# Optimization experiments

Measured on AMD Instinct MI355X. Metric: run time of the kernel, lower is better.

## Reference

```python
import jax, jax.numpy as jnp
import numpy as np

D = 128      # d_single
DP = 64      # d_pair
H = 8        # nhead
DH = D // H  # head dim = 16
DO = 32      # outer proj dim


def layernorm(x, g, b, eps=1e-5):
    mu = jnp.mean(x, axis=-1, keepdims=True)
    var = jnp.var(x, axis=-1, keepdims=True)
    return (x - mu) * jax.lax.rsqrt(var + eps) * g + b


def setup_inputs() -> dict:
    key = jax.random.key(0)
    ks = jax.random.split(key, 16)
    B, L = 2, 320
    s = 0.02
    return {
        "x": jax.random.normal(ks[0], (B, L, D), jnp.float32),
        "z": jax.random.normal(ks[1], (B, L, L, DP), jnp.float32),
        "Wq": jax.random.normal(ks[2], (D, D), jnp.float32) * s,
        "Wk": jax.random.normal(ks[3], (D, D), jnp.float32) * s,
        "Wv": jax.random.normal(ks[4], (D, D), jnp.float32) * s,
        "Wb": jax.random.normal(ks[5], (DP, H), jnp.float32) * s,
        "Wo": jax.random.normal(ks[6], (D, D), jnp.float32) * s,
        "bo": jnp.zeros((D,), jnp.float32),
        "ln1_g": jnp.ones((D,), jnp.float32),
        "ln1_b": jnp.zeros((D,), jnp.float32),
        "W_ffn1": jax.random.normal(ks[7], (D, 4 * D), jnp.float32) * s,
        "b_ffn1": jnp.zeros((4 * D,), jnp.float32),
        "W_ffn2": jax.random.normal(ks[8], (4 * D, D), jnp.float32) * s,
        "b_ffn2": jnp.zeros((D,), jnp.float32),
        "ln2_g": jnp.ones((D,), jnp.float32),
        "ln2_b": jnp.zeros((D,), jnp.float32),
        "Wp1": jax.random.normal(ks[9], (D, DO), jnp.float32) * s,
        "bp1": jnp.zeros((DO,), jnp.float32),
        "Wp2": jax.random.normal(ks[10], (D, DO), jnp.float32) * s,
        "bp2": jnp.zeros((DO,), jnp.float32),
        "Wz": jax.random.normal(ks[11], (DO * DO, DP), jnp.float32) * s,
        "bz": jnp.zeros((DP,), jnp.float32),
        "lnp_g": jnp.ones((DP,), jnp.float32),
        "lnp_b": jnp.zeros((DP,), jnp.float32),
    }


def reference(x, z, Wq, Wk, Wv, Wb, Wo, bo, ln1_g, ln1_b,
              W_ffn1, b_ffn1, W_ffn2, b_ffn2, ln2_g, ln2_b,
              Wp1, bp1, Wp2, bp2, Wz, bz, lnp_g, lnp_b):
    B, L, _ = x.shape
    # --- pair-biased self-attention (dropout = identity in eval) ---
    xn = layernorm(x, ln1_g, ln1_b)
    q = (xn @ Wq).reshape(B, L, H, DH)
    k = (xn @ Wk).reshape(B, L, H, DH)
    v = (xn @ Wv).reshape(B, L, H, DH)
    bias = jnp.einsum('bijp,ph->bhij', z, Wb)                 # [B,H,L,L]
    scores = jnp.einsum('bihd,bjhd->bhij', q, k) / jnp.sqrt(jnp.float32(DH))
    probs = jax.nn.softmax(scores + bias, axis=-1)
    out = jnp.einsum('bhij,bjhd->bihd', probs, v).reshape(B, L, D)
    x = x + out @ Wo + bo
    # --- FFN ---
    xn2 = layernorm(x, ln2_g, ln2_b)
    h = jax.nn.gelu(xn2 @ W_ffn1 + b_ffn1, approximate=False)
    x = x + h @ W_ffn2 + b_ffn2
    # --- outer-product pair update ---
    p1 = x @ Wp1 + bp1                                        # [B,L,32]
    p2 = x @ Wp2 + bp2                                        # [B,L,32]
    # einsum('bic,bjd->bijcd') then flatten(-2) then GEMM with Wz
    Wz4 = Wz.reshape(DO, DO, DP)
    upd = jnp.einsum('bic,bjd,cdp->bijp', p1, p2, Wz4) + bz   # [B,L,L,DP]
    z = layernorm(z + upd, lnp_g, lnp_b)
    return (x, z)
```

## Files before the change

### kernel.cpp

```cpp
#include <hip/hip_runtime.h>
#include <math.h>

#define D   128
#define DP  64
#define H   8
#define DH  16
#define DO  32
#define NB  2
#define L   320
#define NR  (NB * L)

__global__ __launch_bounds__(256) void k1_ln_qkv(
    const float* __restrict__ x, const float* __restrict__ Wq,
    const float* __restrict__ Wk, const float* __restrict__ Wv,
    const float* __restrict__ g, const float* __restrict__ bb,
    float* __restrict__ qkv) {
  __shared__ float xs[2][D];
  __shared__ float stat[2][2];
  const int t = threadIdx.x;
  const int r0 = blockIdx.x * 2;
  const int row = t >> 7, c = t & 127;
  xs[row][c] = x[(r0 + row) * D + c];
  __syncthreads();
  const int w = t >> 6, lane = t & 63;
  if (w < 2) {
    float a = xs[w][lane], cc = xs[w][lane + 64];
    float s = a + cc, s2 = a * a + cc * cc;
#pragma unroll
    for (int off = 32; off >= 1; off >>= 1) {
      s += __shfl_xor(s, off, 64);
      s2 += __shfl_xor(s2, off, 64);
    }
    if (lane == 0) {
      float mu = s * (1.0f / D);
      float var = s2 * (1.0f / D) - mu * mu;
      stat[w][0] = mu;
      stat[w][1] = rsqrtf(var + 1e-5f);
    }
  }
  __syncthreads();
  float xn = (xs[row][c] - stat[row][0]) * stat[row][1] * g[c] + bb[c];
  xs[row][c] = xn;
  __syncthreads();
  float aq = 0, ak = 0, av = 0;
#pragma unroll 4
  for (int k = 0; k < D; ++k) {
    float wq = Wq[k * D + c], wk = Wk[k * D + c], wv = Wv[k * D + c];
    float xv = xs[row][k];
    aq += xv * wq;
    ak += xv * wk;
    av += xv * wv;
  }
  int base = (r0 + row) * 384 + c;
  qkv[base] = aq;
  qkv[base + 128] = ak;
  qkv[base + 256] = av;
}

__global__ __launch_bounds__(256) void k2_bias(
    const float* __restrict__ z, const float* __restrict__ Wb,
    float* __restrict__ bias) {
  __shared__ float zs[64][65];
  __shared__ float wbs[DP * H];
  const int t = threadIdx.x;
  const int jt = blockIdx.x, i = blockIdx.y, b = blockIdx.z;
  const float4* zsrc4 =
      (const float4*)(z + (((size_t)(b * L + i) * L) + jt * 64) * DP);
#pragma unroll
  for (int q = 0; q < 4; ++q) {
    int idx4 = q * 256 + t;
    float4 v = zsrc4[idx4];
    int r = idx4 >> 4, c0 = (idx4 & 15) * 4;
    zs[r][c0] = v.x; zs[r][c0 + 1] = v.y; zs[r][c0 + 2] = v.z; zs[r][c0 + 3] = v.w;
  }
  for (int q = t; q < DP * H; q += 256) wbs[q] = Wb[q];
  __syncthreads();
  const int h0 = t >> 6, j = t & 63;
  float a0 = 0, a1 = 0;
#pragma unroll 8
  for (int p = 0; p < 64; ++p) {
    float zv = zs[j][p];
    a0 += zv * wbs[p * H + h0];
    a1 += zv * wbs[p * H + h0 + 4];
  }
  size_t o0 = (((size_t)(b * H + h0) * L) + i) * L + jt * 64 + j;
  bias[o0] = a0;
  bias[o0 + (size_t)4 * L * L] = a1;
}

__global__ __launch_bounds__(512) void k3_attn(
    const float* __restrict__ qkv, const float* __restrict__ bias,
    float* __restrict__ ao) {
  __shared__ float Ks[L * 17];
  __shared__ float Vs[L * 17];
  __shared__ float qs[8 * DH];
  __shared__ float ps[8][L];
  const int t = threadIdx.x;
  const int i0 = blockIdx.x * 8, h = blockIdx.y, b = blockIdx.z;
  for (int idx = t; idx < L * DH; idx += 512) {
    int j = idx >> 4, d = idx & 15;
    const float* src = qkv + (size_t)(b * L + j) * 384 + h * DH + d;
    Ks[j * 17 + d] = src[128];
    Vs[j * 17 + d] = src[256];
  }
  if (t < 128) {
    int ii = t >> 4, d = t & 15;
    qs[t] = qkv[(size_t)(b * L + i0 + ii) * 384 + h * DH + d] * 0.25f;
  }
  __syncthreads();
  const int w = t >> 6, lane = t & 63;
  const int i = i0 + w;
  const float* brow = bias + (((size_t)(b * H + h) * L) + i) * L;
  float sc[5], m = -1e30f;
#pragma unroll
  for (int it = 0; it < 5; ++it) {
    int j = it * 64 + lane;
    float s = 0;
#pragma unroll
    for (int d = 0; d < DH; ++d) s += qs[w * DH + d] * Ks[j * 17 + d];
    s += brow[j];
    sc[it] = s;
    m = fmaxf(m, s);
  }
#pragma unroll
  for (int off = 32; off >= 1; off >>= 1) m = fmaxf(m, __shfl_xor(m, off, 64));
  float sum = 0;
#pragma unroll
  for (int it = 0; it < 5; ++it) {
    sc[it] = __expf(sc[it] - m);
    sum += sc[it];
  }
#pragma unroll
  for (int off = 32; off >= 1; off >>= 1) sum += __shfl_xor(sum, off, 64);
  float inv = 1.0f / sum;
#pragma unroll
  for (int it = 0; it < 5; ++it) ps[w][it * 64 + lane] = sc[it];
  int d = lane & 15, grp = lane >> 4;
  float acc = 0;
#pragma unroll 4
  for (int j = grp * 80; j < grp * 80 + 80; ++j) acc += ps[w][j] * Vs[j * 17 + d];
  acc += __shfl_xor(acc, 16, 64);
  acc += __shfl_xor(acc, 32, 64);
  if (lane < 16) ao[(size_t)(b * L + i) * D + h * DH + d] = acc * inv;
}

__global__ __launch_bounds__(512) void k45_rowpass(
    const float* __restrict__ x, const float* __restrict__ ao,
    const float* __restrict__ Wo, const float* __restrict__ bo,
    const float* __restrict__ g2, const float* __restrict__ b2,
    const float* __restrict__ W1, const float* __restrict__ bf1,
    const float* __restrict__ W2, const float* __restrict__ bf2,
    const float* __restrict__ Wp1, const float* __restrict__ bp1,
    const float* __restrict__ Wp2, const float* __restrict__ bp2,
    const float* __restrict__ Wz,
    float* __restrict__ out_x, float* __restrict__ p1, float* __restrict__ p2,
    float* __restrict__ T) {
  __shared__ float buf[D];
  __shared__ float x1s[D];
  __shared__ float x2s[D];
  __shared__ float hs[4 * D];
  __shared__ float red[4][D];
  __shared__ float redp[4][64];
  __shared__ float ps_row[64];
  __shared__ float stat[2];
  const int t = threadIdx.x;
  const int row = blockIdx.x;
  const int c = t & 127, q = t >> 7;
  if (t < D) buf[t] = ao[row * D + t];
  __syncthreads();
  {
    float a = 0;
#pragma unroll
    for (int k = q * 32; k < q * 32 + 32; ++k) a += buf[k] * Wo[k * D + c];
    red[q][c] = a;
  }
  __syncthreads();
  if (t < D)
    x1s[t] = x[row * D + t] + red[0][t] + red[1][t] + red[2][t] + red[3][t] + bo[t];
  __syncthreads();
  if (t < 64) {
    float a = x1s[t], bv = x1s[t + 64];
    float s = a + bv, s2 = a * a + bv * bv;
#pragma unroll
    for (int off = 32; off >= 1; off >>= 1) {
      s += __shfl_xor(s, off, 64);
      s2 += __shfl_xor(s2, off, 64);
    }
    if (t == 0) {
      float mu = s * (1.0f / D);
      stat[0] = mu;
      stat[1] = rsqrtf(s2 * (1.0f / D) - mu * mu + 1e-5f);
    }
  }
  __syncthreads();
  if (t < D) buf[t] = (x1s[t] - stat[0]) * stat[1] * g2[t] + b2[t];
  __syncthreads();
  {
    float a = bf1[t];
#pragma unroll 4
    for (int k = 0; k < D; ++k) a += buf[k] * W1[k * 512 + t];
    hs[t] = 0.5f * a * (1.0f + erff(a * 0.70710678118654752f));
  }
  __syncthreads();
  {
    float a = 0;
#pragma unroll 4
    for (int k = q * 128; k < q * 128 + 128; ++k) a += hs[k] * W2[k * D + c];
    red[q][c] = a;
  }
  __syncthreads();
  if (t < D) {
    float x2 = x1s[t] + red[0][t] + red[1][t] + red[2][t] + red[3][t] + bf2[t];
    x2s[t] = x2;
    out_x[row * D + t] = x2;
  }
  __syncthreads();
  if (t < 256) {
    int o = t & 63, q2 = t >> 6;
    const float* W = (o < 32) ? Wp1 : Wp2;
    int cc = o & 31;
    float a = 0;
#pragma unroll
    for (int k = q2 * 32; k < q2 * 32 + 32; ++k) a += x2s[k] * W[k * DO + cc];
    redp[q2][o] = a;
  }
  __syncthreads();
  if (t < 64) {
    float a = redp[0][t] + redp[1][t] + redp[2][t] + redp[3][t] +
              ((t < 32) ? bp1[t] : bp2[t & 31]);
    ps_row[t] = a;
    if (t < 32) p1[row * DO + t] = a;
    else        p2[row * DO + (t & 31)] = a;
  }
  __syncthreads();
  {
#pragma unroll
    for (int qq = 0; qq < 4; ++qq) {
      int idx = qq * 512 + t;
      float a = 0;
#pragma unroll 8
      for (int cc = 0; cc < 32; ++cc) a += ps_row[cc] * Wz[(size_t)cc * 2048 + idx];
      T[(size_t)row * 2048 + idx] = a;
    }
  }
}

__global__ __launch_bounds__(256) void k6_zout(
    const float* __restrict__ z, const float* __restrict__ T,
    const float* __restrict__ p2, const float* __restrict__ bz,
    const float* __restrict__ gp, const float* __restrict__ bp,
    float* __restrict__ zout) {
  __shared__ float p2s[80 * DO];
  const int t = threadIdx.x;
  const int jt = blockIdx.x;
  const int i = blockIdx.y, b = blockIdx.z;
  const size_t row = (size_t)(b * L + i);
  const float* psrc = p2 + ((size_t)b * L + jt * 80) * DO;
#pragma unroll
  for (int qq = 0; qq < 10; ++qq) p2s[qq * 256 + t] = psrc[qq * 256 + t];
  const int w = t >> 6, lane = t & 63;
  float treg[32];
#pragma unroll
  for (int d = 0; d < 32; ++d) treg[d] = T[row * 2048 + d * 64 + lane];
  const float bzv = bz[lane], gv = gp[lane], bv = bp[lane];
  __syncthreads();
  const float* zrow = z + (row * L + (size_t)jt * 80) * DP;
  float* orow = zout + (row * L + (size_t)jt * 80) * DP;
  for (int j0 = 0; j0 < 20; j0 += 2) {
    const int jl0 = w * 20 + j0, jl1 = jl0 + 1;
    const float4* pj0 = (const float4*)&p2s[jl0 * 32];
    const float4* pj1 = (const float4*)&p2s[jl1 * 32];
    float u0 = bzv, u1 = bzv;
#pragma unroll
    for (int dd = 0; dd < 8; ++dd) {
      float4 a = pj0[dd], bq = pj1[dd];
      u0 += a.x * treg[dd * 4] + a.y * treg[dd * 4 + 1] +
            a.z * treg[dd * 4 + 2] + a.w * treg[dd * 4 + 3];
      u1 += bq.x * treg[dd * 4] + bq.y * treg[dd * 4 + 1] +
            bq.z * treg[dd * 4 + 2] + bq.w * treg[dd * 4 + 3];
    }
    float y0 = zrow[jl0 * DP + lane] + u0;
    float y1 = zrow[jl1 * DP + lane] + u1;
    float s0 = y0, q0 = y0 * y0, s1 = y1, q1 = y1 * y1;
#pragma unroll
    for (int off = 32; off >= 1; off >>= 1) {
      s0 += __shfl_xor(s0, off, 64);
      q0 += __shfl_xor(q0, off, 64);
      s1 += __shfl_xor(s1, off, 64);
      q1 += __shfl_xor(q1, off, 64);
    }
    float mu0 = s0 * (1.0f / DP), var0 = q0 * (1.0f / DP) - mu0 * mu0;
    float mu1 = s1 * (1.0f / DP), var1 = q1 * (1.0f / DP) - mu1 * mu1;
    orow[jl0 * DP + lane] = (y0 - mu0) * rsqrtf(var0 + 1e-5f) * gv + bv;
    orow[jl1 * DP + lane] = (y1 - mu1) * rsqrtf(var1 + 1e-5f) * gv + bv;
  }
}

extern "C" void kernel_launch(void* const* d_in, const int* in_sizes, int n_in,
                              void* d_out, int out_size, void* d_ws, size_t ws_size,
                              hipStream_t stream) {
  const float* x      = (const float*)d_in[0];
  const float* z      = (const float*)d_in[1];
  const float* Wq     = (const float*)d_in[2];
  const float* Wk     = (const float*)d_in[3];
  const float* Wv     = (const float*)d_in[4];
  const float* Wb     = (const float*)d_in[5];
  const float* Wo     = (const float*)d_in[6];
  const float* bo     = (const float*)d_in[7];
  const float* ln1_g  = (const float*)d_in[8];
  const float* ln1_b  = (const float*)d_in[9];
  const float* W_ffn1 = (const float*)d_in[10];
  const float* b_ffn1 = (const float*)d_in[11];
  const float* W_ffn2 = (const float*)d_in[12];
  const float* b_ffn2 = (const float*)d_in[13];
  const float* ln2_g  = (const float*)d_in[14];
  const float* ln2_b  = (const float*)d_in[15];
  const float* Wp1    = (const float*)d_in[16];
  const float* bp1    = (const float*)d_in[17];
  const float* Wp2    = (const float*)d_in[18];
  const float* bp2    = (const float*)d_in[19];
  const float* Wz     = (const float*)d_in[20];
  const float* bz     = (const float*)d_in[21];
  const float* lnp_g  = (const float*)d_in[22];
  const float* lnp_b  = (const float*)d_in[23];

  float* ws   = (float*)d_ws;
  float* qkv  = ws;
  float* bias = qkv + 245760;
  float* ao   = bias + 1638400;
  float* p1   = ao + 81920;
  float* p2   = p1 + 20480;
  float* T    = p2 + 20480;

  float* out_x = (float*)d_out;
  float* out_z = out_x + 81920;

  hipLaunchKernelGGL(k1_ln_qkv, dim3(NR / 2), dim3(256), 0, stream,
                     x, Wq, Wk, Wv, ln1_g, ln1_b, qkv);
  hipLaunchKernelGGL(k2_bias, dim3(L / 64, L, NB), dim3(256), 0, stream,
                     z, Wb, bias);
  hipLaunchKernelGGL(k3_attn, dim3(L / 8, H, NB), dim3(512), 0, stream,
                     qkv, bias, ao);
  hipLaunchKernelGGL(k45_rowpass, dim3(NR), dim3(512), 0, stream,
                     x, ao, Wo, bo, ln2_g, ln2_b, W_ffn1, b_ffn1,
                     W_ffn2, b_ffn2, Wp1, bp1, Wp2, bp2, Wz, out_x, p1, p2, T);
  hipLaunchKernelGGL(k6_zout, dim3(4, L, NB), dim3(256), 0, stream,
                     z, T, p2, bz, lnp_g, lnp_b, out_z);
}
```

Before: 244.9 us.

## Vectorize row-pass over two rows, widen attention blocks, add nontemporal z streaming

Several changes land together. The row-pass kernel now processes two rows per block with float4 weight loads, so each weight read from global memory is shared across two rows. The attention kernel handles 16 query rows per 1024-thread block to amortize K/V staging. The z-output kernel processes four pair rows per iteration, prefetches z one group ahead and uses nontemporal loads and stores, and the bias kernel also reads z nontemporally. Launch bounds are tightened, which risks register spills or lower occupancy.

After: 363.6 us. +48.5%, slower.

```diff
diff --git a/kernel.cpp b/kernel.cpp
--- a/kernel.cpp
+++ b/kernel.cpp
@@ -9,6 +9,8 @@
 #define NB  2
 #define L   320
 #define NR  (NB * L)
+
+typedef float f4 __attribute__((ext_vector_type(4)));
 
 __global__ __launch_bounds__(256) void k1_ln_qkv(
     const float* __restrict__ x, const float* __restrict__ Wq,
@@ -64,12 +66,12 @@
   __shared__ float wbs[DP * H];
   const int t = threadIdx.x;
   const int jt = blockIdx.x, i = blockIdx.y, b = blockIdx.z;
-  const float4* zsrc4 =
-      (const float4*)(z + (((size_t)(b * L + i) * L) + jt * 64) * DP);
+  const f4* zsrc4 =
+      (const f4*)(z + (((size_t)(b * L + i) * L) + jt * 64) * DP);
 #pragma unroll
   for (int q = 0; q < 4; ++q) {
     int idx4 = q * 256 + t;
-    float4 v = zsrc4[idx4];
+    f4 v = __builtin_nontemporal_load(zsrc4 + idx4);
     int r = idx4 >> 4, c0 = (idx4 & 15) * 4;
     zs[r][c0] = v.x; zs[r][c0 + 1] = v.y; zs[r][c0 + 2] = v.z; zs[r][c0 + 3] = v.w;
   }
@@ -88,22 +90,22 @@
   bias[o0 + (size_t)4 * L * L] = a1;
 }
 
-__global__ __launch_bounds__(512) void k3_attn(
+__global__ __launch_bounds__(1024, 8) void k3_attn(
     const float* __restrict__ qkv, const float* __restrict__ bias,
     float* __restrict__ ao) {
   __shared__ float Ks[L * 17];
   __shared__ float Vs[L * 17];
-  __shared__ float qs[8 * DH];
-  __shared__ float ps[8][L];
+  __shared__ float qs[16 * DH];
+  __shared__ float ps[16][L];
   const int t = threadIdx.x;
-  const int i0 = blockIdx.x * 8, h = blockIdx.y, b = blockIdx.z;
-  for (int idx = t; idx < L * DH; idx += 512) {
+  const int i0 = blockIdx.x * 16, h = blockIdx.y, b = blockIdx.z;
+  for (int idx = t; idx < L * DH; idx += 1024) {
     int j = idx >> 4, d = idx & 15;
     const float* src = qkv + (size_t)(b * L + j) * 384 + h * DH + d;
     Ks[j * 17 + d] = src[128];
     Vs[j * 17 + d] = src[256];
   }
-  if (t < 128) {
+  if (t < 256) {
     int ii = t >> 4, d = t & 15;
     qs[t] = qkv[(size_t)(b * L + i0 + ii) * 384 + h * DH + d] * 0.25f;
   }
@@ -144,7 +146,7 @@
   if (lane < 16) ao[(size_t)(b * L + i) * D + h * DH + d] = acc * inv;
 }
 
-__global__ __launch_bounds__(512) void k45_rowpass(
+__global__ __launch_bounds__(512, 4) void k45_rowpass(
     const float* __restrict__ x, const float* __restrict__ ao,
     const float* __restrict__ Wo, const float* __restrict__ bo,
     const float* __restrict__ g2, const float* __restrict__ b2,
@@ -155,109 +157,159 @@
     const float* __restrict__ Wz,
     float* __restrict__ out_x, float* __restrict__ p1, float* __restrict__ p2,
     float* __restrict__ T) {
-  __shared__ float buf[D];
-  __shared__ float x1s[D];
-  __shared__ float x2s[D];
-  __shared__ float hs[4 * D];
-  __shared__ float red[4][D];
-  __shared__ float redp[4][64];
-  __shared__ float ps_row[64];
-  __shared__ float stat[2];
+  __shared__ float aos[2][D];
+  __shared__ float x1s[2][D];
+  __shared__ float nrm[2][D];
+  __shared__ float x2s[2][D];
+  __shared__ float hs[2][512];
+  __shared__ __align__(16) float redbuf[4096];
+  __shared__ float ps_row[2][64];
+  __shared__ float stat[2][2];
+  f4* red4 = (f4*)redbuf;
   const int t = threadIdx.x;
-  const int row = blockIdx.x;
-  const int c = t & 127, q = t >> 7;
-  if (t < D) buf[t] = ao[row * D + t];
-  __syncthreads();
-  {
-    float a = 0;
-#pragma unroll
-    for (int k = q * 32; k < q * 32 + 32; ++k) a += buf[k] * Wo[k * D + c];
-    red[q][c] = a;
-  }
-  __syncthreads();
-  if (t < D)
-    x1s[t] = x[row * D + t] + red[0][t] + red[1][t] + red[2][t] + red[3][t] + bo[t];
-  __syncthreads();
-  if (t < 64) {
-    float a = x1s[t], bv = x1s[t + 64];
-    float s = a + bv, s2 = a * a + bv * bv;
+  const int r0 = blockIdx.x * 2;
+  if (t < 256) { int r = t >> 7, c = t & 127; aos[r][c] = ao[(r0 + r) * D + c]; }
+  __syncthreads();
+  {
+    int cg = t & 31, q = t >> 5;
+    f4 a0 = {0, 0, 0, 0}, a1 = {0, 0, 0, 0};
+#pragma unroll
+    for (int k = q * 8; k < q * 8 + 8; ++k) {
+      f4 wv = ((const f4*)(Wo + k * D))[cg];
+      float v0 = aos[0][k], v1 = aos[1][k];
+      a0 += v0 * wv;
+      a1 += v1 * wv;
+    }
+    red4[(q * 2 + 0) * 32 + cg] = a0;
+    red4[(q * 2 + 1) * 32 + cg] = a1;
+  }
+  __syncthreads();
+  if (t < 256) {
+    int r = t >> 7, c = t & 127;
+    float a = x[(r0 + r) * D + c] + bo[c];
+#pragma unroll
+    for (int q = 0; q < 16; ++q) a += redbuf[q * 256 + r * 128 + c];
+    x1s[r][c] = a;
+  }
+  __syncthreads();
+  if (t < 128) {
+    int w = t >> 6, lane = t & 63;
+    float a = x1s[w][lane], cc = x1s[w][lane + 64];
+    float s = a + cc, s2 = a * a + cc * cc;
 #pragma unroll
     for (int off = 32; off >= 1; off >>= 1) {
       s += __shfl_xor(s, off, 64);
       s2 += __shfl_xor(s2, off, 64);
     }
-    if (t == 0) {
+    if (lane == 0) {
       float mu = s * (1.0f / D);
-      stat[0] = mu;
-      stat[1] = rsqrtf(s2 * (1.0f / D) - mu * mu + 1e-5f);
-    }
-  }
-  __syncthreads();
-  if (t < D) buf[t] = (x1s[t] - stat[0]) * stat[1] * g2[t] + b2[t];
-  __syncthreads();
-  {
-    float a = bf1[t];
+      stat[w][0] = mu;
+      stat[w][1] = rsqrtf(s2 * (1.0f / D) - mu * mu + 1e-5f);
+    }
+  }
+  __syncthreads();
+  if (t < 256) {
+    int r = t >> 7, c = t & 127;
+    nrm[r][c] = (x1s[r][c] - stat[r][0]) * stat[r][1] * g2[c] + b2[c];
+  }
+  __syncthreads();
+  {
+    int cg = t & 127, q = t >> 7;
+    f4 a0 = {0, 0, 0, 0}, a1 = {0, 0, 0, 0};
 #pragma unroll 4
-    for (int k = 0; k < D; ++k) a += buf[k] * W1[k * 512 + t];
-    hs[t] = 0.5f * a * (1.0f + erff(a * 0.70710678118654752f));
-  }
-  __syncthreads();
-  {
-    float a = 0;
+    for (int k = q * 32; k < q * 32 + 32; ++k) {
+      f4 wv = ((const f4*)(W1 + k * 512))[cg];
+      float v0 = nrm[0][k], v1 = nrm[1][k];
+      a0 += v0 * wv;
+      a1 += v1 * wv;
+    }
+    red4[q * 256 + 0 * 128 + cg] = a0;
+    red4[q * 256 + 1 * 128 + cg] = a1;
+  }
+  __syncthreads();
+  {
+#pragma unroll
+    for (int r = 0; r < 2; ++r) {
+      float a = bf1[t];
+#pragma unroll
+      for (int q = 0; q < 4; ++q) a += redbuf[q * 1024 + r * 512 + t];
+      hs[r][t] = 0.5f * a * (1.0f + erff(a * 0.70710678118654752f));
+    }
+  }
+  __syncthreads();
+  {
+    int cg = t & 31, q = t >> 5;
+    f4 a0 = {0, 0, 0, 0}, a1 = {0, 0, 0, 0};
 #pragma unroll 4
-    for (int k = q * 128; k < q * 128 + 128; ++k) a += hs[k] * W2[k * D + c];
-    red[q][c] = a;
-  }
-  __syncthreads();
-  if (t < D) {
-    float x2 = x1s[t] + red[0][t] + red[1][t] + red[2][t] + red[3][t] + bf2[t];
-    x2s[t] = x2;
-    out_x[row * D + t] = x2;
+    for (int k = q * 32; k < q * 32 + 32; ++k) {
+      f4 wv = ((const f4*)(W2 + k * D))[cg];
+      float v0 = hs[0][k], v1 = hs[1][k];
+      a0 += v0 * wv;
+      a1 += v1 * wv;
+    }
+    red4[(q * 2 + 0) * 32 + cg] = a0;
+    red4[(q * 2 + 1) * 32 + cg] = a1;
   }
   __syncthreads();
   if (t < 256) {
-    int o = t & 63, q2 = t >> 6;
+    int r = t >> 7, c = t & 127;
+    float a = x1s[r][c] + bf2[c];
+#pragma unroll
+    for (int q = 0; q < 16; ++q) a += redbuf[q * 256 + r * 128 + c];
+    x2s[r][c] = a;
+    out_x[(r0 + r) * D + c] = a;
+  }
+  __syncthreads();
+  {
+    int o = t & 63, r = (t >> 6) & 1, q = t >> 7;
     const float* W = (o < 32) ? Wp1 : Wp2;
     int cc = o & 31;
     float a = 0;
 #pragma unroll
-    for (int k = q2 * 32; k < q2 * 32 + 32; ++k) a += x2s[k] * W[k * DO + cc];
-    redp[q2][o] = a;
-  }
-  __syncthreads();
-  if (t < 64) {
-    float a = redp[0][t] + redp[1][t] + redp[2][t] + redp[3][t] +
-              ((t < 32) ? bp1[t] : bp2[t & 31]);
-    ps_row[t] = a;
-    if (t < 32) p1[row * DO + t] = a;
-    else        p2[row * DO + (t & 31)] = a;
-  }
-  __syncthreads();
-  {
-#pragma unroll
-    for (int qq = 0; qq < 4; ++qq) {
-      int idx = qq * 512 + t;
-      float a = 0;
+    for (int k = q * 32; k < q * 32 + 32; ++k) a += x2s[r][k] * W[k * DO + cc];
+    redbuf[t] = a;
+  }
+  __syncthreads();
+  if (t < 128) {
+    int r = t >> 6, o = t & 63;
+    float a = redbuf[0 * 128 + r * 64 + o] + redbuf[1 * 128 + r * 64 + o] +
+              redbuf[2 * 128 + r * 64 + o] + redbuf[3 * 128 + r * 64 + o] +
+              ((o < 32) ? bp1[o] : bp2[o & 31]);
+    ps_row[r][o] = a;
+    if (o < 32) p1[(r0 + r) * DO + o] = a;
+    else        p2[(r0 + r) * DO + (o & 31)] = a;
+  }
+  __syncthreads();
+  {
+    const f4* Wz4 = (const f4*)Wz;
+    f4 a0 = {0, 0, 0, 0}, a1 = {0, 0, 0, 0};
 #pragma unroll 8
-      for (int cc = 0; cc < 32; ++cc) a += ps_row[cc] * Wz[(size_t)cc * 2048 + idx];
-      T[(size_t)row * 2048 + idx] = a;
-    }
-  }
-}
-
-__global__ __launch_bounds__(256) void k6_zout(
+    for (int cc = 0; cc < 32; ++cc) {
+      f4 wv = Wz4[cc * 512 + t];
+      float v0 = ps_row[0][cc], v1 = ps_row[1][cc];
+      a0 += v0 * wv;
+      a1 += v1 * wv;
+    }
+    ((f4*)T)[(size_t)(r0 + 0) * 512 + t] = a0;
+    ((f4*)T)[(size_t)(r0 + 1) * 512 + t] = a1;
+  }
+}
+
+__global__ __launch_bounds__(256, 5) void k6_zout(
     const float* __restrict__ z, const float* __restrict__ T,
     const float* __restrict__ p2, const float* __restrict__ bz,
     const float* __restrict__ gp, const float* __restrict__ bp,
     float* __restrict__ zout) {
-  __shared__ float p2s[80 * DO];
+  __shared__ __align__(16) float p2s[80 * DO];
   const int t = threadIdx.x;
   const int jt = blockIdx.x;
   const int i = blockIdx.y, b = blockIdx.z;
   const size_t row = (size_t)(b * L + i);
-  const float* psrc = p2 + ((size_t)b * L + jt * 80) * DO;
-#pragma unroll
-  for (int qq = 0; qq < 10; ++qq) p2s[qq * 256 + t] = psrc[qq * 256 + t];
+  {
+    const f4* psrc4 = (const f4*)(p2 + ((size_t)b * L + jt * 80) * DO);
+    f4* p2s4 = (f4*)p2s;
+    for (int q = t; q < 640; q += 256) p2s4[q] = psrc4[q];
+  }
   const int w = t >> 6, lane = t & 63;
   float treg[32];
 #pragma unroll
@@ -266,33 +318,57 @@
   __syncthreads();
   const float* zrow = z + (row * L + (size_t)jt * 80) * DP;
   float* orow = zout + (row * L + (size_t)jt * 80) * DP;
-  for (int j0 = 0; j0 < 20; j0 += 2) {
-    const int jl0 = w * 20 + j0, jl1 = jl0 + 1;
-    const float4* pj0 = (const float4*)&p2s[jl0 * 32];
-    const float4* pj1 = (const float4*)&p2s[jl1 * 32];
-    float u0 = bzv, u1 = bzv;
+  const int jb = w * 20;
+  float zv0 = __builtin_nontemporal_load(&zrow[(jb + 0) * DP + lane]);
+  float zv1 = __builtin_nontemporal_load(&zrow[(jb + 1) * DP + lane]);
+  float zv2 = __builtin_nontemporal_load(&zrow[(jb + 2) * DP + lane]);
+  float zv3 = __builtin_nontemporal_load(&zrow[(jb + 3) * DP + lane]);
+#pragma unroll
+  for (int g = 0; g < 5; ++g) {
+    const int j0 = jb + g * 4;
+    const f4* pj0 = (const f4*)&p2s[(j0 + 0) * DO];
+    const f4* pj1 = (const f4*)&p2s[(j0 + 1) * DO];
+    const f4* pj2 = (const f4*)&p2s[(j0 + 2) * DO];
+    const f4* pj3 = (const f4*)&p2s[(j0 + 3) * DO];
+    float u0 = bzv, u1 = bzv, u2 = bzv, u3 = bzv;
 #pragma unroll
     for (int dd = 0; dd < 8; ++dd) {
-      float4 a = pj0[dd], bq = pj1[dd];
-      u0 += a.x * treg[dd * 4] + a.y * treg[dd * 4 + 1] +
-            a.z * treg[dd * 4 + 2] + a.w * treg[dd * 4 + 3];
-      u1 += bq.x * treg[dd * 4] + bq.y * treg[dd * 4 + 1] +
-            bq.z * treg[dd * 4 + 2] + bq.w * treg[dd * 4 + 3];
-    }
-    float y0 = zrow[jl0 * DP + lane] + u0;
-    float y1 = zrow[jl1 * DP + lane] + u1;
+      float t0 = treg[dd * 4], t1 = treg[dd * 4 + 1];
+      float t2 = treg[dd * 4 + 2], t3 = treg[dd * 4 + 3];
+      f4 a0 = pj0[dd], a1 = pj1[dd], a2 = pj2[dd], a3 = pj3[dd];
+      u0 += a0.x * t0 + a0.y * t1 + a0.z * t2 + a0.w * t3;
+      u1 += a1.x * t0 + a1.y * t1 + a1.z * t2 + a1.w * t3;
+      u2 += a2.x * t0 + a2.y * t1 + a2.z * t2 + a2.w * t3;
+      u3 += a3.x * t0 + a3.y * t1 + a3.z * t2 + a3.w * t3;
+    }
+    float y0 = zv0 + u0, y1 = zv1 + u1, y2 = zv2 + u2, y3 = zv3 + u3;
+    if (g < 4) {
+      zv0 = __builtin_nontemporal_load(&zrow[(j0 + 4) * DP + lane]);
+      zv1 = __builtin_nontemporal_load(&zrow[(j0 + 5) * DP + lane]);
+      zv2 = __builtin_nontemporal_load(&zrow[(j0 + 6) * DP + lane]);
+      zv3 = __builtin_nontemporal_load(&zrow[(j0 + 7) * DP + lane]);
+    }
     float s0 = y0, q0 = y0 * y0, s1 = y1, q1 = y1 * y1;
+    float s2 = y2, q2 = y2 * y2, s3 = y3, q3 = y3 * y3;
 #pragma unroll
     for (int off = 32; off >= 1; off >>= 1) {
-      s0 += __shfl_xor(s0, off, 64);
-      q0 += __shfl_xor(q0, off, 64);
-      s1 += __shfl_xor(s1, off, 64);
-      q1 += __shfl_xor(q1, off, 64);
-    }
-    float mu0 = s0 * (1.0f / DP), var0 = q0 * (1.0f / DP) - mu0 * mu0;
-    float mu1 = s1 * (1.0f / DP), var1 = q1 * (1.0f / DP) - mu1 * mu1;
-    orow[jl0 * DP + lane] = (y0 - mu0) * rsqrtf(var0 + 1e-5f) * gv + bv;
-    orow[jl1 * DP + lane] = (y1 - mu1) * rsqrtf(var1 + 1e-5f) * gv + bv;
+      s0 += __shfl_xor(s0, off, 64); q0 += __shfl_xor(q0, off, 64);
+      s1 += __shfl_xor(s1, off, 64); q1 += __shfl_xor(q1, off, 64);
+      s2 += __shfl_xor(s2, off, 64); q2 += __shfl_xor(q2, off, 64);
+      s3 += __shfl_xor(s3, off, 64); q3 += __shfl_xor(q3, off, 64);
+    }
+    float mu0 = s0 * (1.0f / DP), va0 = q0 * (1.0f / DP) - mu0 * mu0;
+    float mu1 = s1 * (1.0f / DP), va1 = q1 * (1.0f / DP) - mu1 * mu1;
+    float mu2 = s2 * (1.0f / DP), va2 = q2 * (1.0f / DP) - mu2 * mu2;
+    float mu3 = s3 * (1.0f / DP), va3 = q3 * (1.0f / DP) - mu3 * mu3;
+    __builtin_nontemporal_store((y0 - mu0) * rsqrtf(va0 + 1e-5f) * gv + bv,
+                                &orow[(j0 + 0) * DP + lane]);
+    __builtin_nontemporal_store((y1 - mu1) * rsqrtf(va1 + 1e-5f) * gv + bv,
+                                &orow[(j0 + 1) * DP + lane]);
+    __builtin_nontemporal_store((y2 - mu2) * rsqrtf(va2 + 1e-5f) * gv + bv,
+                                &orow[(j0 + 2) * DP + lane]);
+    __builtin_nontemporal_store((y3 - mu3) * rsqrtf(va3 + 1e-5f) * gv + bv,
+                                &orow[(j0 + 3) * DP + lane]);
   }
 }
 
@@ -339,9 +415,9 @@
                      x, Wq, Wk, Wv, ln1_g, ln1_b, qkv);
   hipLaunchKernelGGL(k2_bias, dim3(L / 64, L, NB), dim3(256), 0, stream,
                      z, Wb, bias);
-  hipLaunchKernelGGL(k3_attn, dim3(L / 8, H, NB), dim3(512), 0, stream,
+  hipLaunchKernelGGL(k3_attn, dim3(L / 16, H, NB), dim3(1024), 0, stream,
                      qkv, bias, ao);
-  hipLaunchKernelGGL(k45_rowpass, dim3(NR), dim3(512), 0, stream,
+  hipLaunchKernelGGL(k45_rowpass, dim3(NR / 2), dim3(512), 0, stream,
                      x, ao, Wo, bo, ln2_g, ln2_b, W_ffn1, b_ffn1,
                      W_ffn2, b_ffn2, Wp1, bp1, Wp2, bp2, Wz, out_x, p1, p2, T);
   hipLaunchKernelGGL(k6_zout, dim3(4, L, NB), dim3(256), 0, stream,
```
